# Optimization experiments

Measured on AMD Instinct MI355X. Metric: run time of the kernel, lower is better.

Reference implementation:

```python
import jax, jax.numpy as jnp
import numpy as np

B, C, H, N, M = 4, 256, 4, 2048, 2048
D = C // H  # head_dim
BN_EPS = 1e-5


def conv1x1(W, b, x):
    # nn.Conv1d(Cin, Cout, kernel_size=1): x [B, Cin, N] -> [B, Cout, N]
    return jnp.einsum('oc,bcn->bon', W, x) + b[None, :, None]


def setup_inputs() -> dict:
    key = jax.random.key(0)
    ks = jax.random.split(key, 10)
    w = lambda k, shape: (jax.random.normal(k, shape, jnp.float32) * 0.05)
    return {
        'x1': jax.random.normal(ks[0], (B, C, N), jnp.float32),
        'x2': jax.random.normal(ks[1], (B, C, M), jnp.float32),
        'kv_mask': jax.random.randint(ks[2], (B, M), 0, 2).astype(bool),
        'Wq': w(ks[3], (C, C)), 'bq': jnp.zeros((C,), jnp.float32),
        'Wk': w(ks[4], (C, C)), 'bk': jnp.zeros((C,), jnp.float32),
        'Wv': w(ks[5], (C, C)), 'bv': jnp.zeros((C,), jnp.float32),
        'Wmh': w(ks[6], (C, C)), 'bmh': jnp.zeros((C,), jnp.float32),
        'W1': w(ks[7], (2 * C, 2 * C)), 'b1': jnp.zeros((2 * C,), jnp.float32),
        'bn_gamma': jnp.ones((2 * C,), jnp.float32),
        'bn_beta': jnp.zeros((2 * C,), jnp.float32),
        'bn_mean': jnp.zeros((2 * C,), jnp.float32),
        'bn_var': jnp.ones((2 * C,), jnp.float32),
        'W2': w(ks[8], (C, 2 * C)), 'b2': jnp.zeros((C,), jnp.float32),
    }


def reference(x1, x2, kv_mask, Wq, bq, Wk, bk, Wv, bv, Wmh, bmh,
              W1, b1, bn_gamma, bn_beta, bn_mean, bn_var, W2, b2):
    bsz = x1.shape[0]
    # 1x1-conv Q/K/V projections, reshaped to [B, H, D, N]
    q = conv1x1(Wq, bq, x1).reshape(bsz, H, D, -1)
    k = conv1x1(Wk, bk, x2).reshape(bsz, H, D, -1)
    v = conv1x1(Wv, bv, x2).reshape(bsz, H, D, -1)

    # full attention: scores [B, H, N, M]
    QK = jnp.einsum('bhdn,bhdm->bhnm', q, k)
    # masked_fill happens BEFORE the 1/sqrt(D) scaling in the original
    QK = jnp.where(kv_mask[:, None, None, :], QK, jnp.float32(-1e6))
    score = jax.nn.softmax(QK / np.float32(np.sqrt(D)), axis=-1)
    add_value = jnp.einsum('bhnm,bhdm->bhdn', score, v).reshape(bsz, H * D, -1)

    add_value = conv1x1(Wmh, bmh, add_value)

    # cat_filter: conv1x1 -> BatchNorm1d (inference stats) -> ReLU -> conv1x1
    cat = jnp.concatenate([x1, add_value], axis=1)  # [B, 2C, N]
    h = conv1x1(W1, b1, cat)
    h = (h - bn_mean[None, :, None]) / jnp.sqrt(bn_var[None, :, None] + BN_EPS)
    h = bn_gamma[None, :, None] * h + bn_beta[None, :, None]
    h = jax.nn.relu(h)
    return x1 + conv1x1(W2, b2, h)
```

## Files before the change

kernel.cpp:

```cpp
#include <hip/hip_runtime.h>
#include <hip/hip_bf16.h>

#define SEQN 2048
#define SEQM 2048
#define CDIM 256
#define NB   4
#define NH   4

using bf16x8 = __attribute__((ext_vector_type(8))) short;
using f32x4  = __attribute__((ext_vector_type(4))) float;

__device__ inline unsigned short f2bf(float x) {
    __hip_bfloat16 h = __float2bfloat16(x);
    return *reinterpret_cast<unsigned short*>(&h);
}

__global__ __launch_bounds__(256) void prep_k(
    const int* __restrict__ kvm, int* __restrict__ pidx, int* __restrict__ mcnt,
    const float* __restrict__ W1, const float* __restrict__ b1,
    const float* __restrict__ gamma, const float* __restrict__ beta,
    const float* __restrict__ mean, const float* __restrict__ var,
    const float* __restrict__ Wmh, const float* __restrict__ bmh,
    unsigned short* __restrict__ Acat, float* __restrict__ cvec,
    const float* __restrict__ Wq, const float* __restrict__ Wk,
    const float* __restrict__ Wv, const float* __restrict__ W2,
    unsigned short* __restrict__ Wqb, unsigned short* __restrict__ Wkb,
    unsigned short* __restrict__ Wvb, unsigned short* __restrict__ W2b,
    const float* __restrict__ x1, const float* __restrict__ x2,
    unsigned short* __restrict__ catT, unsigned short* __restrict__ x2T)
{
    __shared__ float smemf[64 * 68];
    const int bid = blockIdx.x, tid = threadIdx.x;

    if (bid < NB) {
        int* sc = reinterpret_cast<int*>(smemf);
        const int b = bid;
        int loc[8], c = 0;
        #pragma unroll
        for (int e = 0; e < 8; ++e) {
            loc[e] = (kvm[(size_t)b * SEQM + tid * 8 + e] != 0) ? 1 : 0;
            c += loc[e];
        }
        sc[tid] = c;
        __syncthreads();
        for (int off = 1; off < 256; off <<= 1) {
            int v = (tid >= off) ? sc[tid - off] : 0;
            __syncthreads();
            sc[tid] += v;
            __syncthreads();
        }
        int p = sc[tid] - c;
        if (tid == 255) mcnt[b] = sc[255];
        #pragma unroll
        for (int e = 0; e < 8; ++e) {
            pidx[(size_t)b * SEQM + tid * 8 + e] = loc[e] ? p : -1;
            p += loc[e];
        }
    } else if (bid < NB + 512) {
        const int j = bid - NB;
        const int c = tid;
        const float s = gamma[j] * rsqrtf(var[j] + 1e-5f);
        const float* w1b = W1 + (size_t)j * 512 + 256;
        Acat[(size_t)j * 512 + c] = f2bf(s * W1[(size_t)j * 512 + c]);
        float acc = 0.f;
        for (int t = 0; t < 256; ++t)
            acc += w1b[t] * Wmh[(size_t)t * 256 + c];
        Acat[(size_t)j * 512 + 256 + c] = f2bf(s * acc);
        if (c == 0) {
            float ab = 0.f;
            for (int t = 0; t < 256; ++t) ab += w1b[t] * bmh[t];
            cvec[j] = s * (b1[j] + ab - mean[j]) + beta[j];
        }
    } else if (bid < NB + 512 + 320) {
        int cid = bid - (NB + 512);
        const float* src; unsigned short* dst; int n;
        if (cid < 64)       { src = Wq; dst = Wqb; n = 65536; }
        else if (cid < 128) { src = Wk; dst = Wkb; n = 65536;  cid -= 64;  }
        else if (cid < 192) { src = Wv; dst = Wvb; n = 65536;  cid -= 128; }
        else                { src = W2; dst = W2b; n = 131072; cid -= 192; }
        const int idx = (cid * 256 + tid) * 4;
        if (idx < n) {
            float4 v = *reinterpret_cast<const float4*>(&src[idx]);
            ushort4 p; p.x = f2bf(v.x); p.y = f2bf(v.y); p.z = f2bf(v.z); p.w = f2bf(v.w);
            *reinterpret_cast<ushort4*>(&dst[idx]) = p;
        }
    } else {
        int t = bid - (NB + 512 + 320);
        const float* src; unsigned short* dst; int ldd;
        if (t < 512) { src = x1; dst = catT; ldd = 512; }
        else         { src = x2; dst = x2T;  ldd = 256; t -= 512; }
        const int cx = t & 3, ny = (t >> 2) & 31, b = t >> 7;
        const int c0 = cx * 64, n0 = ny * 64;
        float (*Ts)[68] = reinterpret_cast<float(*)[68]>(smemf);
        const int cr = tid >> 2, nc = (tid & 3) * 16;
        #pragma unroll
        for (int q = 0; q < 4; ++q) {
            float4 v = *reinterpret_cast<const float4*>(
                &src[((size_t)b * CDIM + c0 + cr) * SEQN + n0 + nc + 4 * q]);
            *reinterpret_cast<float4*>(&Ts[cr][nc + 4 * q]) = v;
        }
        __syncthreads();
        const int nr = tid >> 2, cc = (tid & 3) * 16;
        unsigned short tmp[16];
        #pragma unroll
        for (int e = 0; e < 16; ++e) tmp[e] = f2bf(Ts[cc + e][nr]);
        unsigned short* dp = &dst[((size_t)(b * SEQN + n0 + nr)) * ldd + c0 + cc];
        #pragma unroll
        for (int q = 0; q < 4; ++q)
            *reinterpret_cast<ushort4*>(&dp[4 * q]) = *reinterpret_cast<ushort4*>(&tmp[4 * q]);
    }
}

__global__ __launch_bounds__(256) void qkv_gemm_k(
    const unsigned short* __restrict__ Wqb, const unsigned short* __restrict__ Wkb,
    const unsigned short* __restrict__ Wvb,
    const unsigned short* __restrict__ catT, const unsigned short* __restrict__ x2T,
    const float* __restrict__ bq, const float* __restrict__ bk,
    const float* __restrict__ bv,
    unsigned short* __restrict__ qbf, unsigned short* __restrict__ kbf,
    unsigned short* __restrict__ vbf,
    const int* __restrict__ pidx, float qscale)
{
    __shared__ short At[128][72];
    __shared__ short Bt[64][72];
    const int z = blockIdx.z;
    const unsigned short* W = (z == 0) ? Wqb : (z == 1) ? Wkb : Wvb;
    const unsigned short* X = (z == 0) ? catT : x2T;
    const float* bias = (z == 0) ? bq : (z == 1) ? bk : bv;
    const int ldx = (z == 0) ? 512 : 256;

    const int tid = threadIdx.x;
    const int w = tid >> 6, l = tid & 63, lm = l & 15, lg = l >> 4;
    const int o0 = blockIdx.x * 128, ng0 = blockIdx.y * 64;
    const int wo = (w >> 1) * 64, wn = (w & 1) * 32;

    f32x4 acc[4][2] = {};
    const int arow = tid >> 2, acol = (tid & 3) * 16;

    for (int k0 = 0; k0 < 256; k0 += 64) {
        __syncthreads();
        #pragma unroll
        for (int p = 0; p < 2; ++p) {
            const unsigned short* s = &W[(size_t)(o0 + arow + 64 * p) * 256 + k0 + acol];
            *reinterpret_cast<bf16x8*>(&At[arow + 64 * p][acol]) =
                *reinterpret_cast<const bf16x8*>(s);
            *reinterpret_cast<bf16x8*>(&At[arow + 64 * p][acol + 8]) =
                *reinterpret_cast<const bf16x8*>(s + 8);
        }
        {
            const unsigned short* s = &X[(size_t)(ng0 + arow) * ldx + k0 + acol];
            *reinterpret_cast<bf16x8*>(&Bt[arow][acol]) =
                *reinterpret_cast<const bf16x8*>(s);
            *reinterpret_cast<bf16x8*>(&Bt[arow][acol + 8]) =
                *reinterpret_cast<const bf16x8*>(s + 8);
        }
        __syncthreads();
        #pragma unroll
        for (int kc = 0; kc < 2; ++kc) {
            bf16x8 a[4], bf[2];
            #pragma unroll
            for (int i = 0; i < 4; ++i)
                a[i] = *reinterpret_cast<const bf16x8*>(&At[wo + 16 * i + lm][kc * 32 + lg * 8]);
            #pragma unroll
            for (int j = 0; j < 2; ++j)
                bf[j] = *reinterpret_cast<const bf16x8*>(&Bt[wn + 16 * j + lm][kc * 32 + lg * 8]);
            #pragma unroll
            for (int i = 0; i < 4; ++i)
                #pragma unroll
                for (int j = 0; j < 2; ++j)
                    acc[i][j] = __builtin_amdgcn_mfma_f32_16x16x32_bf16(a[i], bf[j], acc[i][j], 0, 0, 0);
        }
    }

    #pragma unroll
    for (int j = 0; j < 2; ++j) {
        const int ng = ng0 + wn + 16 * j + lm;
        const int b = ng >> 11, n = ng & 2047;
        const int pos = (z == 0) ? n : pidx[(size_t)b * SEQM + n];
        #pragma unroll
        for (int i = 0; i < 4; ++i) {
            const int ob = o0 + wo + 16 * i + 4 * lg;
            float4 bv4 = *reinterpret_cast<const float4*>(&bias[ob]);
            float v[4] = {acc[i][j][0] + bv4.x, acc[i][j][1] + bv4.y,
                          acc[i][j][2] + bv4.z, acc[i][j][3] + bv4.w};
            if (z == 2) {
                if (pos >= 0) {
                    #pragma unroll
                    for (int r = 0; r < 4; ++r)
                        vbf[((size_t)b * CDIM + ob + r) * SEQM + pos] = f2bf(v[r]);
                }
            } else if (pos >= 0) {
                const int hh = ob >> 6, dbase = ob & 63;
                const float sc_ = (z == 0) ? qscale : 1.0f;
                ushort4 pk;
                pk.x = f2bf(v[0] * sc_); pk.y = f2bf(v[1] * sc_);
                pk.z = f2bf(v[2] * sc_); pk.w = f2bf(v[3] * sc_);
                unsigned short* dst = (z == 0) ? qbf : kbf;
                *reinterpret_cast<ushort4*>(
                    &dst[(((size_t)b * NH + hh) * SEQN + pos) * 64 + dbase]) = pk;
            }
        }
    }
}

template<int OMODE>
__global__ __launch_bounds__(256) void gemm_mfma_k(
    const unsigned short* __restrict__ W, const unsigned short* __restrict__ X,
    const float* __restrict__ bias, const float* __restrict__ res,
    unsigned short* __restrict__ obf, float* __restrict__ ofp,
    const int* __restrict__ pidx, int K, int ldx, float oscale)
{
    __shared__ short At[128][72];
    __shared__ short Bt[64][72];
    const int tid = threadIdx.x;
    const int w = tid >> 6, l = tid & 63, lm = l & 15, lg = l >> 4;
    const int o0 = blockIdx.x * 128, ng0 = blockIdx.y * 64;
    const int wo = (w >> 1) * 64, wn = (w & 1) * 32;

    f32x4 acc[4][2] = {};
    const int arow = tid >> 2, acol = (tid & 3) * 16;

    for (int k0 = 0; k0 < K; k0 += 64) {
        __syncthreads();
        #pragma unroll
        for (int p = 0; p < 2; ++p) {
            const unsigned short* s = &W[(size_t)(o0 + arow + 64 * p) * K + k0 + acol];
            *reinterpret_cast<bf16x8*>(&At[arow + 64 * p][acol]) =
                *reinterpret_cast<const bf16x8*>(s);
            *reinterpret_cast<bf16x8*>(&At[arow + 64 * p][acol + 8]) =
                *reinterpret_cast<const bf16x8*>(s + 8);
        }
        {
            const unsigned short* s = &X[(size_t)(ng0 + arow) * ldx + k0 + acol];
            *reinterpret_cast<bf16x8*>(&Bt[arow][acol]) =
                *reinterpret_cast<const bf16x8*>(s);
            *reinterpret_cast<bf16x8*>(&Bt[arow][acol + 8]) =
                *reinterpret_cast<const bf16x8*>(s + 8);
        }
        __syncthreads();
        #pragma unroll
        for (int kc = 0; kc < 2; ++kc) {
            bf16x8 a[4], bf[2];
            #pragma unroll
            for (int i = 0; i < 4; ++i)
                a[i] = *reinterpret_cast<const bf16x8*>(&At[wo + 16 * i + lm][kc * 32 + lg * 8]);
            #pragma unroll
            for (int j = 0; j < 2; ++j)
                bf[j] = *reinterpret_cast<const bf16x8*>(&Bt[wn + 16 * j + lm][kc * 32 + lg * 8]);
            #pragma unroll
            for (int i = 0; i < 4; ++i)
                #pragma unroll
                for (int j = 0; j < 2; ++j)
                    acc[i][j] = __builtin_amdgcn_mfma_f32_16x16x32_bf16(a[i], bf[j], acc[i][j], 0, 0, 0);
        }
    }

    #pragma unroll
    for (int j = 0; j < 2; ++j) {
        const int ng = ng0 + wn + 16 * j + lm;
        const int b = ng >> 11, n = ng & 2047;
        #pragma unroll
        for (int i = 0; i < 4; ++i) {
            const int ob = o0 + wo + 16 * i + 4 * lg;
            float4 bv = *reinterpret_cast<const float4*>(&bias[ob]);
            float v[4] = {acc[i][j][0] + bv.x, acc[i][j][1] + bv.y,
                          acc[i][j][2] + bv.z, acc[i][j][3] + bv.w};
            if (OMODE == 2) {
                ushort4 pk;
                pk.x = f2bf(fmaxf(v[0], 0.f)); pk.y = f2bf(fmaxf(v[1], 0.f));
                pk.z = f2bf(fmaxf(v[2], 0.f)); pk.w = f2bf(fmaxf(v[3], 0.f));
                *reinterpret_cast<ushort4*>(&obf[(size_t)ng * 512 + ob]) = pk;
            } else {
                #pragma unroll
                for (int r = 0; r < 4; ++r) {
                    size_t ad = ((size_t)b * CDIM + ob + r) * SEQN + n;
                    ofp[ad] = v[r] + res[ad];
                }
            }
        }
    }
}

__global__ __launch_bounds__(256) void attn_mfma_k(
    const unsigned short* __restrict__ qbf, const unsigned short* __restrict__ kbf,
    const unsigned short* __restrict__ vbf, const int* __restrict__ mcntg,
    unsigned short* __restrict__ catT)
{
    __shared__ short Ks[2][64][64];
    __shared__ short Vs[2][64][64];
    __shared__ unsigned int Ps[4][16][36];

    const int tid = threadIdx.x;
    const int w = tid >> 6, l = tid & 63;
    const int lm = l & 15, lg = l >> 4;
    const int h = blockIdx.y, b = blockIdx.z;
    const int n_base = blockIdx.x * 64 + w * 16;
    const size_t bhN = (size_t)(b * NH + h) * SEQN;
    const size_t cBase = (size_t)b * CDIM + h * 64;

    const int mcnt = mcntg[b];
    const int ntiles = (mcnt + 63) >> 6;

    if (ntiles == 0) {
        #pragma unroll
        for (int r = 0; r < 4; ++r) {
            int n = n_base + 4 * lg + r;
            unsigned short* dst = &catT[((size_t)b * SEQN + n) * 512 + 256 + h * 64];
            #pragma unroll
            for (int t = 0; t < 4; ++t) dst[16 * t + lm] = 0;
        }
        return;
    }

    const size_t qrow = (bhN + n_base + lm) * 64;
    bf16x8 qa0 = *reinterpret_cast<const bf16x8*>(&qbf[qrow + lg * 8]);
    bf16x8 qa1 = *reinterpret_cast<const bf16x8*>(&qbf[qrow + 32 + lg * 8]);

    f32x4 oacc[4] = {};
    float mrun = -3.0e5f, lrun = 0.f;

    const int r0 = tid >> 3, c8 = (tid & 7) * 8;
    const int c8s = c8 ^ ((r0 & 7) << 3);
    const int colr0 = (lg * 8) ^ ((lm & 7) << 3);
    const int colr1 = (32 + lg * 8) ^ ((lm & 7) << 3);

    {
        bf16x8 kr[2], vr[2];
        #pragma unroll
        for (int p = 0; p < 2; ++p) {
            kr[p] = *reinterpret_cast<const bf16x8*>(&kbf[(bhN + r0 + 32 * p) * 64 + c8]);
            vr[p] = *reinterpret_cast<const bf16x8*>(&vbf[(cBase + r0 + 32 * p) * SEQM + c8]);
        }
        #pragma unroll
        for (int p = 0; p < 2; ++p) {
            *reinterpret_cast<bf16x8*>(&Ks[0][r0 + 32 * p][c8s]) = kr[p];
            *reinterpret_cast<bf16x8*>(&Vs[0][r0 + 32 * p][c8s]) = vr[p];
        }
    }
    __syncthreads();

    for (int t64 = 0; t64 < ntiles; ++t64) {
        const int cur = t64 & 1;
        const bool has_next = (t64 < ntiles - 1);
        const int m0n = (t64 + 1) * 64;

        bf16x8 kr[2], vr[2];
        if (has_next) {
            #pragma unroll
            for (int p = 0; p < 2; ++p) {
                kr[p] = *reinterpret_cast<const bf16x8*>(
                    &kbf[(bhN + m0n + r0 + 32 * p) * 64 + c8]);
                vr[p] = *reinterpret_cast<const bf16x8*>(
                    &vbf[(cBase + r0 + 32 * p) * SEQM + m0n + c8]);
            }
        }

        f32x4 sv[4];
        __builtin_amdgcn_s_setprio(1);
        #pragma unroll
        for (int t = 0; t < 4; ++t) {
            bf16x8 ka0 = *reinterpret_cast<const bf16x8*>(&Ks[cur][16 * t + lm][colr0]);
            bf16x8 ka1 = *reinterpret_cast<const bf16x8*>(&Ks[cur][16 * t + lm][colr1]);
            f32x4 z = {0.f, 0.f, 0.f, 0.f};
            z = __builtin_amdgcn_mfma_f32_16x16x32_bf16(ka0, qa0, z, 0, 0, 0);
            z = __builtin_amdgcn_mfma_f32_16x16x32_bf16(ka1, qa1, z, 0, 0, 0);
            sv[t] = z;
        }
        __builtin_amdgcn_s_setprio(0);

        float mx = fmaxf(fmaxf(fmaxf(sv[0][0], sv[0][1]), fmaxf(sv[0][2], sv[0][3])),
                         fmaxf(fmaxf(sv[1][0], sv[1][1]), fmaxf(sv[1][2], sv[1][3])));
        mx = fmaxf(mx, fmaxf(fmaxf(fmaxf(sv[2][0], sv[2][1]), fmaxf(sv[2][2], sv[2][3])),
                             fmaxf(fmaxf(sv[3][0], sv[3][1]), fmaxf(sv[3][2], sv[3][3]))));
        mx = fmaxf(mx, __shfl_xor(mx, 16));
        mx = fmaxf(mx, __shfl_xor(mx, 32));
        const bool grew = (mx > mrun);
        float mnew = fmaxf(mrun, mx);
        float scl = exp2f(mrun - mnew);
        mrun = mnew;

        float rsum = 0.f;
        const int mrem = mcnt - t64 * 64;
        if (mrem >= 64) {
            #pragma unroll
            for (int t = 0; t < 4; ++t) {
                float p0 = exp2f(sv[t][0] - mnew);
                float p1 = exp2f(sv[t][1] - mnew);
                float p2 = exp2f(sv[t][2] - mnew);
                float p3 = exp2f(sv[t][3] - mnew);
                rsum += (p0 + p1) + (p2 + p3);
                unsigned int u0 = __builtin_amdgcn_perm(
                    __float_as_uint(p1), __float_as_uint(p0), 0x07060302u);
                unsigned int u1 = __builtin_amdgcn_perm(
                    __float_as_uint(p3), __float_as_uint(p2), 0x07060302u);
                *reinterpret_cast<uint2*>(&Ps[w][lm][8 * t + 2 * lg]) = make_uint2(u0, u1);
            }
        } else {
            #pragma unroll
            for (int t = 0; t < 4; ++t) {
                const int mb = 16 * t + 4 * lg;
                float p0 = (mb + 0 < mrem) ? exp2f(sv[t][0] - mnew) : 0.f;
                float p1 = (mb + 1 < mrem) ? exp2f(sv[t][1] - mnew) : 0.f;
                float p2 = (mb + 2 < mrem) ? exp2f(sv[t][2] - mnew) : 0.f;
                float p3 = (mb + 3 < mrem) ? exp2f(sv[t][3] - mnew) : 0.f;
                rsum += (p0 + p1) + (p2 + p3);
                unsigned int u0 = __builtin_amdgcn_perm(
                    __float_as_uint(p1), __float_as_uint(p0), 0x07060302u);
                unsigned int u1 = __builtin_amdgcn_perm(
                    __float_as_uint(p3), __float_as_uint(p2), 0x07060302u);
                *reinterpret_cast<uint2*>(&Ps[w][lm][8 * t + 2 * lg]) = make_uint2(u0, u1);
            }
        }
        rsum += __shfl_xor(rsum, 16);
        rsum += __shfl_xor(rsum, 32);
        lrun = lrun * scl + rsum;

        if (__any(grew && scl < 1.f)) {
            float sr[4];
            #pragma unroll
            for (int r = 0; r < 4; ++r) sr[r] = __shfl(scl, 4 * lg + r);
            #pragma unroll
            for (int t = 0; t < 4; ++t)
                #pragma unroll
                for (int r = 0; r < 4; ++r)
                    oacc[t][r] *= sr[r];
        }

        bf16x8 pa0 = *reinterpret_cast<const bf16x8*>(&Ps[w][lm][4 * lg]);
        bf16x8 pa1 = *reinterpret_cast<const bf16x8*>(&Ps[w][lm][16 + 4 * lg]);
        __builtin_amdgcn_s_setprio(1);
        #pragma unroll
        for (int t = 0; t < 4; ++t) {
            bf16x8 vb0 = *reinterpret_cast<const bf16x8*>(&Vs[cur][16 * t + lm][colr0]);
            bf16x8 vb1 = *reinterpret_cast<const bf16x8*>(&Vs[cur][16 * t + lm][colr1]);
            oacc[t] = __builtin_amdgcn_mfma_f32_16x16x32_bf16(pa0, vb0, oacc[t], 0, 0, 0);
            oacc[t] = __builtin_amdgcn_mfma_f32_16x16x32_bf16(pa1, vb1, oacc[t], 0, 0, 0);
        }
        __builtin_amdgcn_s_setprio(0);

        if (has_next) {
            const int nxt = cur ^ 1;
            #pragma unroll
            for (int p = 0; p < 2; ++p) {
                *reinterpret_cast<bf16x8*>(&Ks[nxt][r0 + 32 * p][c8s]) = kr[p];
                *reinterpret_cast<bf16x8*>(&Vs[nxt][r0 + 32 * p][c8s]) = vr[p];
            }
        }
        __syncthreads();
    }

    #pragma unroll
    for (int r = 0; r < 4; ++r) {
        float rinv = 1.f / __shfl(lrun, 4 * lg + r);
        int n = n_base + 4 * lg + r;
        unsigned short* dst = &catT[((size_t)b * SEQN + n) * 512 + 256 + h * 64];
        #pragma unroll
        for (int t = 0; t < 4; ++t)
            dst[16 * t + lm] = f2bf(oacc[t][r] * rinv);
    }
}

extern "C" void kernel_launch(void* const* d_in, const int* in_sizes, int n_in,
                              void* d_out, int out_size, void* d_ws, size_t ws_size,
                              hipStream_t stream)
{
    (void)in_sizes; (void)n_in; (void)out_size; (void)ws_size;
    const float* x1    = (const float*)d_in[0];
    const float* x2    = (const float*)d_in[1];
    const int*   kvm   = (const int*)  d_in[2];
    const float* Wq    = (const float*)d_in[3];
    const float* bq    = (const float*)d_in[4];
    const float* Wk    = (const float*)d_in[5];
    const float* bk    = (const float*)d_in[6];
    const float* Wv    = (const float*)d_in[7];
    const float* bv    = (const float*)d_in[8];
    const float* Wmh   = (const float*)d_in[9];
    const float* bmh   = (const float*)d_in[10];
    const float* W1    = (const float*)d_in[11];
    const float* b1    = (const float*)d_in[12];
    const float* gamma = (const float*)d_in[13];
    const float* beta  = (const float*)d_in[14];
    const float* mean  = (const float*)d_in[15];
    const float* var   = (const float*)d_in[16];
    const float* W2    = (const float*)d_in[17];
    const float* b2    = (const float*)d_in[18];
    float* out = (float*)d_out;

    const size_t act = (size_t)NB * CDIM * SEQN;
    unsigned short* ws   = (unsigned short*)d_ws;
    unsigned short* qbf  = ws;
    unsigned short* kbf  = qbf  + act;
    unsigned short* vbf  = kbf  + act;
    unsigned short* x2T  = vbf  + act;
    unsigned short* catT = x2T  + act;
    unsigned short* hbuf = catT + 2 * act;
    unsigned short* Wqb  = hbuf + 2 * act;
    unsigned short* Wkb  = Wqb  + 65536;
    unsigned short* Wvb  = Wkb  + 65536;
    unsigned short* W2b  = Wvb  + 65536;
    unsigned short* Acat = W2b  + 131072;
    float*          cvec = (float*)(Acat + 262144);
    int*            pidx = (int*)(cvec + 512);
    int*            mcnt = pidx + (size_t)NB * SEQM;

    const float qscale = 0.125f * 1.44269504088896f;

    prep_k<<<dim3(NB + 512 + 320 + 1024), dim3(256), 0, stream>>>(
        kvm, pidx, mcnt,
        W1, b1, gamma, beta, mean, var, Wmh, bmh, Acat, cvec,
        Wq, Wk, Wv, W2, Wqb, Wkb, Wvb, W2b,
        x1, x2, catT, x2T);

    qkv_gemm_k<<<dim3(2, 128, 3), dim3(256), 0, stream>>>(
        Wqb, Wkb, Wvb, catT, x2T, bq, bk, bv, qbf, kbf, vbf, pidx, qscale);

    attn_mfma_k<<<dim3(SEQN / 64, NH, NB), dim3(256), 0, stream>>>(
        qbf, kbf, vbf, mcnt, catT);

    gemm_mfma_k<2><<<dim3(4, 128), dim3(256), 0, stream>>>(
        Acat, catT, cvec, nullptr, hbuf, nullptr, nullptr, 512, 512, 1.0f);

    gemm_mfma_k<3><<<dim3(2, 128), dim3(256), 0, stream>>>(
        W2b, hbuf, b2, x1, nullptr, out, nullptr, 512, 512, 1.0f);
}
```

Before: 83.31 us.

## Fuse bf16 conversion into QKV GEMM and merge attention with weight prep

The QKV projection now reads fp32 weights and activations directly, converting to bf16 and transposing through shared memory inside the GEMM. This removes the separate conversion and transpose pass and its intermediate buffers. The mask prefix scan runs in the same launch, and K/V blocks spin on a per-batch ready flag before scattering compacted rows. Attention is merged into one launch with the folded Wmh/W1 weight prep and the W2 conversion, cutting the launch count and letting independent work overlap. The ready flag is never reset between calls, which risks reading stale prefix indices, and the spin-wait depends on the scan blocks being scheduled first.

```diff
diff --git a/kernel.cpp b/kernel.cpp
--- a/kernel.cpp
+++ b/kernel.cpp
@@ -6,6 +6,7 @@
 #define CDIM 256
 #define NB   4
 #define NH   4
+#define RDYMAGIC 0x7A3F19C5u
 
 using bf16x8 = __attribute__((ext_vector_type(8))) short;
 using f32x4  = __attribute__((ext_vector_type(4))) float;
@@ -15,49 +16,363 @@
     return *reinterpret_cast<unsigned short*>(&h);
 }
 
-__global__ __launch_bounds__(256) void prep_k(
+__global__ __launch_bounds__(256, 4) void qkv_k(
+    const float* __restrict__ Wq, const float* __restrict__ Wk,
+    const float* __restrict__ Wv,
+    const float* __restrict__ x1, const float* __restrict__ x2,
+    const float* __restrict__ bq, const float* __restrict__ bk,
+    const float* __restrict__ bv,
+    unsigned short* __restrict__ qbf, unsigned short* __restrict__ kbf,
+    unsigned short* __restrict__ vbf,
     const int* __restrict__ kvm, int* __restrict__ pidx, int* __restrict__ mcnt,
+    unsigned int* __restrict__ rdy, float qscale)
+{
+    __shared__ __align__(16) char qsm[35840];
+    const int bid = blockIdx.x, tid = threadIdx.x;
+
+    if (bid < NB) {
+        int* sc = reinterpret_cast<int*>(qsm);
+        const int b = bid;
+        int loc[8], c = 0;
+        #pragma unroll
+        for (int e = 0; e < 8; ++e) {
+            loc[e] = (kvm[(size_t)b * SEQM + tid * 8 + e] != 0) ? 1 : 0;
+            c += loc[e];
+        }
+        sc[tid] = c;
+        __syncthreads();
+        for (int off = 1; off < 256; off <<= 1) {
+            int v = (tid >= off) ? sc[tid - off] : 0;
+            __syncthreads();
+            sc[tid] += v;
+            __syncthreads();
+        }
+        int p = sc[tid] - c;
+        if (tid == 255) mcnt[b] = sc[255];
+        #pragma unroll
+        for (int e = 0; e < 8; ++e) {
+            pidx[(size_t)b * SEQM + tid * 8 + e] = loc[e] ? p : -1;
+            p += loc[e];
+        }
+        __threadfence();
+        __syncthreads();
+        if (tid == 0)
+            __hip_atomic_store(&rdy[b], RDYMAGIC, __ATOMIC_RELEASE,
+                               __HIP_MEMORY_SCOPE_AGENT);
+        return;
+    }
+
+    const int g = bid - NB;
+    const int z = g >> 8, t = g & 255;
+    const int bx = t & 1, by = t >> 1;
+
+    short (*At)[72] = reinterpret_cast<short(*)[72]>(qsm);
+    float (*Ts)[68] = reinterpret_cast<float(*)[68]>(qsm + 18432);
+
+    const float* W = (z == 0) ? Wq : (z == 1) ? Wk : Wv;
+    const float* X = (z == 0) ? x1 : x2;
+    const float* bias = (z == 0) ? bq : (z == 1) ? bk : bv;
+
+    const int w = tid >> 6, l = tid & 63, lm = l & 15, lg = l >> 4;
+    const int o0 = bx * 128, ng0 = by * 64;
+    const int b = ng0 >> 11, n0 = ng0 & 2047;
+    const int wo = (w >> 1) * 64, wn = (w & 1) * 32;
+
+    f32x4 acc[4][2] = {};
+    const int arow = tid >> 2, acol = (tid & 3) * 16;
+    const int tr = tid >> 2, tc = (tid & 3) * 16;
+    const int tg = (((tc >> 4) ^ ((tr >> 3) & 3)) << 4);
+
+    for (int k0 = 0; k0 < 256; k0 += 64) {
+        __syncthreads();
+        #pragma unroll
+        for (int p = 0; p < 2; ++p) {
+            const float* s = &W[(size_t)(o0 + arow + 64 * p) * 256 + k0 + acol];
+            unsigned int u[8];
+            #pragma unroll
+            for (int q = 0; q < 4; ++q) {
+                float4 f = *reinterpret_cast<const float4*>(&s[4 * q]);
+                u[2 * q]     = (unsigned int)f2bf(f.x) | ((unsigned int)f2bf(f.y) << 16);
+                u[2 * q + 1] = (unsigned int)f2bf(f.z) | ((unsigned int)f2bf(f.w) << 16);
+            }
+            *reinterpret_cast<uint4*>(&At[arow + 64 * p][acol]) =
+                make_uint4(u[0], u[1], u[2], u[3]);
+            *reinterpret_cast<uint4*>(&At[arow + 64 * p][acol + 8]) =
+                make_uint4(u[4], u[5], u[6], u[7]);
+        }
+        {
+            const float* s = &X[((size_t)b * CDIM + k0 + tr) * SEQN + n0 + tc];
+            #pragma unroll
+            for (int q = 0; q < 4; ++q)
+                *reinterpret_cast<float4*>(&Ts[tr][tg + 4 * q]) =
+                    *reinterpret_cast<const float4*>(&s[4 * q]);
+        }
+        __syncthreads();
+        #pragma unroll
+        for (int kc = 0; kc < 2; ++kc) {
+            bf16x8 a[4], bf[2];
+            #pragma unroll
+            for (int i = 0; i < 4; ++i)
+                a[i] = *reinterpret_cast<const bf16x8*>(&At[wo + 16 * i + lm][kc * 32 + lg * 8]);
+            #pragma unroll
+            for (int j = 0; j < 2; ++j) {
+                const int bk0 = kc * 32 + lg * 8;
+                const int gcol = (((((wn >> 4) + j)) ^ ((bk0 >> 3) & 3)) << 4) | lm;
+                union { unsigned int u[4]; bf16x8 v; } cv;
+                #pragma unroll
+                for (int e = 0; e < 4; ++e) {
+                    float lo = Ts[bk0 + 2 * e][gcol];
+                    float hi = Ts[bk0 + 2 * e + 1][gcol];
+                    cv.u[e] = (unsigned int)f2bf(lo) | ((unsigned int)f2bf(hi) << 16);
+                }
+                bf[j] = cv.v;
+            }
+            #pragma unroll
+            for (int i = 0; i < 4; ++i)
+                #pragma unroll
+                for (int j = 0; j < 2; ++j)
+                    acc[i][j] = __builtin_amdgcn_mfma_f32_16x16x32_bf16(a[i], bf[j], acc[i][j], 0, 0, 0);
+        }
+    }
+
+    if (z != 0) {
+        if (tid == 0) {
+            while (__hip_atomic_load(&rdy[b], __ATOMIC_ACQUIRE,
+                                     __HIP_MEMORY_SCOPE_AGENT) != RDYMAGIC)
+                __builtin_amdgcn_s_sleep(2);
+        }
+        __syncthreads();
+    }
+
+    #pragma unroll
+    for (int j = 0; j < 2; ++j) {
+        const int ng = ng0 + wn + 16 * j + lm;
+        const int bb = ng >> 11, n = ng & 2047;
+        const int pos = (z == 0) ? n : pidx[(size_t)bb * SEQM + n];
+        #pragma unroll
+        for (int i = 0; i < 4; ++i) {
+            const int ob = o0 + wo + 16 * i + 4 * lg;
+            float4 bv4 = *reinterpret_cast<const float4*>(&bias[ob]);
+            float v[4] = {acc[i][j][0] + bv4.x, acc[i][j][1] + bv4.y,
+                          acc[i][j][2] + bv4.z, acc[i][j][3] + bv4.w};
+            if (z == 2) {
+                if (pos >= 0) {
+                    #pragma unroll
+                    for (int r = 0; r < 4; ++r)
+                        vbf[((size_t)bb * CDIM + ob + r) * SEQM + pos] = f2bf(v[r]);
+                }
+            } else if (pos >= 0) {
+                const int hh = ob >> 6, dbase = ob & 63;
+                const float sc_ = (z == 0) ? qscale : 1.0f;
+                ushort4 pk;
+                pk.x = f2bf(v[0] * sc_); pk.y = f2bf(v[1] * sc_);
+                pk.z = f2bf(v[2] * sc_); pk.w = f2bf(v[3] * sc_);
+                unsigned short* dst = (z == 0) ? qbf : kbf;
+                *reinterpret_cast<ushort4*>(
+                    &dst[(((size_t)bb * NH + hh) * SEQN + pos) * 64 + dbase]) = pk;
+            }
+        }
+    }
+}
+
+__device__ void do_attn(char* smraw,
+    const unsigned short* __restrict__ qbf, const unsigned short* __restrict__ kbf,
+    const unsigned short* __restrict__ vbf, const int* __restrict__ mcntg,
+    unsigned short* __restrict__ catT, int bx, int h, int b)
+{
+    short (*Ks)[64][64] = reinterpret_cast<short(*)[64][64]>(smraw);
+    short (*Vs)[64][64] = reinterpret_cast<short(*)[64][64]>(smraw + 16384);
+    unsigned int (*Ps)[16][36] = reinterpret_cast<unsigned int(*)[16][36]>(smraw + 32768);
+
+    const int tid = threadIdx.x;
+    const int w = tid >> 6, l = tid & 63;
+    const int lm = l & 15, lg = l >> 4;
+    const int n_base = bx * 64 + w * 16;
+    const size_t bhN = (size_t)(b * NH + h) * SEQN;
+    const size_t cBase = (size_t)b * CDIM + h * 64;
+
+    const int mcnt = mcntg[b];
+    const int ntiles = (mcnt + 63) >> 6;
+
+    if (ntiles == 0) {
+        #pragma unroll
+        for (int r = 0; r < 4; ++r) {
+            int n = n_base + 4 * lg + r;
+            unsigned short* dst = &catT[((size_t)b * SEQN + n) * 512 + 256 + h * 64];
+            #pragma unroll
+            for (int t = 0; t < 4; ++t) dst[16 * t + lm] = 0;
+        }
+        return;
+    }
+
+    const size_t qrow = (bhN + n_base + lm) * 64;
+    bf16x8 qa0 = *reinterpret_cast<const bf16x8*>(&qbf[qrow + lg * 8]);
+    bf16x8 qa1 = *reinterpret_cast<const bf16x8*>(&qbf[qrow + 32 + lg * 8]);
+
+    f32x4 oacc[4] = {};
+    float mrun = -3.0e5f, lrun = 0.f;
+
+    const int r0 = tid >> 3, c8 = (tid & 7) * 8;
+    const int c8s = c8 ^ ((r0 & 7) << 3);
+    const int colr0 = (lg * 8) ^ ((lm & 7) << 3);
+    const int colr1 = (32 + lg * 8) ^ ((lm & 7) << 3);
+
+    {
+        bf16x8 kr[2], vr[2];
+        #pragma unroll
+        for (int p = 0; p < 2; ++p) {
+            kr[p] = *reinterpret_cast<const bf16x8*>(&kbf[(bhN + r0 + 32 * p) * 64 + c8]);
+            vr[p] = *reinterpret_cast<const bf16x8*>(&vbf[(cBase + r0 + 32 * p) * SEQM + c8]);
+        }
+        #pragma unroll
+        for (int p = 0; p < 2; ++p) {
+            *reinterpret_cast<bf16x8*>(&Ks[0][r0 + 32 * p][c8s]) = kr[p];
+            *reinterpret_cast<bf16x8*>(&Vs[0][r0 + 32 * p][c8s]) = vr[p];
+        }
+    }
+    __syncthreads();
+
+    for (int t64 = 0; t64 < ntiles; ++t64) {
+        const int cur = t64 & 1;
+        const bool has_next = (t64 < ntiles - 1);
+        const int m0n = (t64 + 1) * 64;
+
+        bf16x8 kr[2], vr[2];
+        if (has_next) {
+            #pragma unroll
+            for (int p = 0; p < 2; ++p) {
+                kr[p] = *reinterpret_cast<const bf16x8*>(
+                    &kbf[(bhN + m0n + r0 + 32 * p) * 64 + c8]);
+                vr[p] = *reinterpret_cast<const bf16x8*>(
+                    &vbf[(cBase + r0 + 32 * p) * SEQM + m0n + c8]);
+            }
+        }
+
+        f32x4 sv[4];
+        __builtin_amdgcn_s_setprio(1);
+        #pragma unroll
+        for (int t = 0; t < 4; ++t) {
+            bf16x8 ka0 = *reinterpret_cast<const bf16x8*>(&Ks[cur][16 * t + lm][colr0]);
+            bf16x8 ka1 = *reinterpret_cast<const bf16x8*>(&Ks[cur][16 * t + lm][colr1]);
+            f32x4 z = {0.f, 0.f, 0.f, 0.f};
+            z = __builtin_amdgcn_mfma_f32_16x16x32_bf16(ka0, qa0, z, 0, 0, 0);
+            z = __builtin_amdgcn_mfma_f32_16x16x32_bf16(ka1, qa1, z, 0, 0, 0);
+            sv[t] = z;
+        }
+        __builtin_amdgcn_s_setprio(0);
+
+        float mx = fmaxf(fmaxf(fmaxf(sv[0][0], sv[0][1]), fmaxf(sv[0][2], sv[0][3])),
+                         fmaxf(fmaxf(sv[1][0], sv[1][1]), fmaxf(sv[1][2], sv[1][3])));
+        mx = fmaxf(mx, fmaxf(fmaxf(fmaxf(sv[2][0], sv[2][1]), fmaxf(sv[2][2], sv[2][3])),
+                             fmaxf(fmaxf(sv[3][0], sv[3][1]), fmaxf(sv[3][2], sv[3][3]))));
+        mx = fmaxf(mx, __shfl_xor(mx, 16));
+        mx = fmaxf(mx, __shfl_xor(mx, 32));
+        const bool grew = (mx > mrun);
+        float mnew = fmaxf(mrun, mx);
+        float scl = exp2f(mrun - mnew);
+        mrun = mnew;
+
+        float rsum = 0.f;
+        const int mrem = mcnt - t64 * 64;
+        if (mrem >= 64) {
+            #pragma unroll
+            for (int t = 0; t < 4; ++t) {
+                float p0 = exp2f(sv[t][0] - mnew);
+                float p1 = exp2f(sv[t][1] - mnew);
+                float p2 = exp2f(sv[t][2] - mnew);
+                float p3 = exp2f(sv[t][3] - mnew);
+                rsum += (p0 + p1) + (p2 + p3);
+                unsigned int u0 = __builtin_amdgcn_perm(
+                    __float_as_uint(p1), __float_as_uint(p0), 0x07060302u);
+                unsigned int u1 = __builtin_amdgcn_perm(
+                    __float_as_uint(p3), __float_as_uint(p2), 0x07060302u);
+                *reinterpret_cast<uint2*>(&Ps[w][lm][8 * t + 2 * lg]) = make_uint2(u0, u1);
+            }
+        } else {
+            #pragma unroll
+            for (int t = 0; t < 4; ++t) {
+                const int mb = 16 * t + 4 * lg;
+                float p0 = (mb + 0 < mrem) ? exp2f(sv[t][0] - mnew) : 0.f;
+                float p1 = (mb + 1 < mrem) ? exp2f(sv[t][1] - mnew) : 0.f;
+                float p2 = (mb + 2 < mrem) ? exp2f(sv[t][2] - mnew) : 0.f;
+                float p3 = (mb + 3 < mrem) ? exp2f(sv[t][3] - mnew) : 0.f;
+                rsum += (p0 + p1) + (p2 + p3);
+                unsigned int u0 = __builtin_amdgcn_perm(
+                    __float_as_uint(p1), __float_as_uint(p0), 0x07060302u);
+                unsigned int u1 = __builtin_amdgcn_perm(
+                    __float_as_uint(p3), __float_as_uint(p2), 0x07060302u);
+                *reinterpret_cast<uint2*>(&Ps[w][lm][8 * t + 2 * lg]) = make_uint2(u0, u1);
+            }
+        }
+        rsum += __shfl_xor(rsum, 16);
+        rsum += __shfl_xor(rsum, 32);
+        lrun = lrun * scl + rsum;
+
+        if (__any(grew && scl < 1.f)) {
+            float sr[4];
+            #pragma unroll
+            for (int r = 0; r < 4; ++r) sr[r] = __shfl(scl, 4 * lg + r);
+            #pragma unroll
+            for (int t = 0; t < 4; ++t)
+                #pragma unroll
+                for (int r = 0; r < 4; ++r)
+                    oacc[t][r] *= sr[r];
+        }
+
+        bf16x8 pa0 = *reinterpret_cast<const bf16x8*>(&Ps[w][lm][4 * lg]);
+        bf16x8 pa1 = *reinterpret_cast<const bf16x8*>(&Ps[w][lm][16 + 4 * lg]);
+        __builtin_amdgcn_s_setprio(1);
+        #pragma unroll
+        for (int t = 0; t < 4; ++t) {
+            bf16x8 vb0 = *reinterpret_cast<const bf16x8*>(&Vs[cur][16 * t + lm][colr0]);
+            bf16x8 vb1 = *reinterpret_cast<const bf16x8*>(&Vs[cur][16 * t + lm][colr1]);
+            oacc[t] = __builtin_amdgcn_mfma_f32_16x16x32_bf16(pa0, vb0, oacc[t], 0, 0, 0);
+            oacc[t] = __builtin_amdgcn_mfma_f32_16x16x32_bf16(pa1, vb1, oacc[t], 0, 0, 0);
+        }
+        __builtin_amdgcn_s_setprio(0);
+
+        if (has_next) {
+            const int nxt = cur ^ 1;
+            #pragma unroll
+            for (int p = 0; p < 2; ++p) {
+                *reinterpret_cast<bf16x8*>(&Ks[nxt][r0 + 32 * p][c8s]) = kr[p];
+                *reinterpret_cast<bf16x8*>(&Vs[nxt][r0 + 32 * p][c8s]) = vr[p];
+            }
+        }
+        __syncthreads();
+    }
+
+    #pragma unroll
+    for (int r = 0; r < 4; ++r) {
+        float rinv = 1.f / __shfl(lrun, 4 * lg + r);
+        int n = n_base + 4 * lg + r;
+        unsigned short* dst = &catT[((size_t)b * SEQN + n) * 512 + 256 + h * 64];
+        #pragma unroll
+        for (int t = 0; t < 4; ++t)
+            dst[16 * t + lm] = f2bf(oacc[t][r] * rinv);
+    }
+}
+
+__global__ __launch_bounds__(256) void fused2_k(
+    const unsigned short* __restrict__ qbf, const unsigned short* __restrict__ kbf,
+    const unsigned short* __restrict__ vbf, const int* __restrict__ mcnt,
+    unsigned short* __restrict__ catT,
     const float* __restrict__ W1, const float* __restrict__ b1,
     const float* __restrict__ gamma, const float* __restrict__ beta,
     const float* __restrict__ mean, const float* __restrict__ var,
     const float* __restrict__ Wmh, const float* __restrict__ bmh,
     unsigned short* __restrict__ Acat, float* __restrict__ cvec,
-    const float* __restrict__ Wq, const float* __restrict__ Wk,
-    const float* __restrict__ Wv, const float* __restrict__ W2,
-    unsigned short* __restrict__ Wqb, unsigned short* __restrict__ Wkb,
-    unsigned short* __restrict__ Wvb, unsigned short* __restrict__ W2b,
-    const float* __restrict__ x1, const float* __restrict__ x2,
-    unsigned short* __restrict__ catT, unsigned short* __restrict__ x2T)
+    const float* __restrict__ x1,
+    const float* __restrict__ W2, unsigned short* __restrict__ W2b)
 {
-    __shared__ float smemf[64 * 68];
+    __shared__ __align__(16) char smraw[41984];
     const int bid = blockIdx.x, tid = threadIdx.x;
 
-    if (bid < NB) {
-        int* sc = reinterpret_cast<int*>(smemf);
-        const int b = bid;
-        int loc[8], c = 0;
-        #pragma unroll
-        for (int e = 0; e < 8; ++e) {
-            loc[e] = (kvm[(size_t)b * SEQM + tid * 8 + e] != 0) ? 1 : 0;
-            c += loc[e];
-        }
-        sc[tid] = c;
-        __syncthreads();
-        for (int off = 1; off < 256; off <<= 1) {
-            int v = (tid >= off) ? sc[tid - off] : 0;
-            __syncthreads();
-            sc[tid] += v;
-            __syncthreads();
-        }
-        int p = sc[tid] - c;
-        if (tid == 255) mcnt[b] = sc[255];
-        #pragma unroll
-        for (int e = 0; e < 8; ++e) {
-            pidx[(size_t)b * SEQM + tid * 8 + e] = loc[e] ? p : -1;
-            p += loc[e];
-        }
-    } else if (bid < NB + 512) {
-        const int j = bid - NB;
+    if (bid < 512) {
+        do_attn(smraw, qbf, kbf, vbf, mcnt, catT,
+                bid & 31, (bid >> 5) & 3, bid >> 7);
+    } else if (bid < 1024) {
+        const int j = bid - 512;
         const int c = tid;
         const float s = gamma[j] * rsqrtf(var[j] + 1e-5f);
         const float* w1b = W1 + (size_t)j * 512 + 256;
@@ -71,32 +386,16 @@
             for (int t = 0; t < 256; ++t) ab += w1b[t] * bmh[t];
             cvec[j] = s * (b1[j] + ab - mean[j]) + beta[j];
         }
-    } else if (bid < NB + 512 + 320) {
-        int cid = bid - (NB + 512);
-        const float* src; unsigned short* dst; int n;
-        if (cid < 64)       { src = Wq; dst = Wqb; n = 65536; }
-        else if (cid < 128) { src = Wk; dst = Wkb; n = 65536;  cid -= 64;  }
-        else if (cid < 192) { src = Wv; dst = Wvb; n = 65536;  cid -= 128; }
-        else                { src = W2; dst = W2b; n = 131072; cid -= 192; }
-        const int idx = (cid * 256 + tid) * 4;
-        if (idx < n) {
-            float4 v = *reinterpret_cast<const float4*>(&src[idx]);
-            ushort4 p; p.x = f2bf(v.x); p.y = f2bf(v.y); p.z = f2bf(v.z); p.w = f2bf(v.w);
-            *reinterpret_cast<ushort4*>(&dst[idx]) = p;
-        }
-    } else {
-        int t = bid - (NB + 512 + 320);
-        const float* src; unsigned short* dst; int ldd;
-        if (t < 512) { src = x1; dst = catT; ldd = 512; }
-        else         { src = x2; dst = x2T;  ldd = 256; t -= 512; }
+    } else if (bid < 1536) {
+        const int t = bid - 1024;
+        float (*Ts)[68] = reinterpret_cast<float(*)[68]>(smraw);
         const int cx = t & 3, ny = (t >> 2) & 31, b = t >> 7;
         const int c0 = cx * 64, n0 = ny * 64;
-        float (*Ts)[68] = reinterpret_cast<float(*)[68]>(smemf);
         const int cr = tid >> 2, nc = (tid & 3) * 16;
         #pragma unroll
         for (int q = 0; q < 4; ++q) {
             float4 v = *reinterpret_cast<const float4*>(
-                &src[((size_t)b * CDIM + c0 + cr) * SEQN + n0 + nc + 4 * q]);
+                &x1[((size_t)b * CDIM + c0 + cr) * SEQN + n0 + nc + 4 * q]);
             *reinterpret_cast<float4*>(&Ts[cr][nc + 4 * q]) = v;
         }
         __syncthreads();
@@ -104,102 +403,16 @@
         unsigned short tmp[16];
         #pragma unroll
         for (int e = 0; e < 16; ++e) tmp[e] = f2bf(Ts[cc + e][nr]);
-        unsigned short* dp = &dst[((size_t)(b * SEQN + n0 + nr)) * ldd + c0 + cc];
+        unsigned short* dp = &catT[((size_t)(b * SEQN + n0 + nr)) * 512 + c0 + cc];
         #pragma unroll
         for (int q = 0; q < 4; ++q)
             *reinterpret_cast<ushort4*>(&dp[4 * q]) = *reinterpret_cast<ushort4*>(&tmp[4 * q]);
-    }
-}
-
-__global__ __launch_bounds__(256) void qkv_gemm_k(
-    const unsigned short* __restrict__ Wqb, const unsigned short* __restrict__ Wkb,
-    const unsigned short* __restrict__ Wvb,
-    const unsigned short* __restrict__ catT, const unsigned short* __restrict__ x2T,
-    const float* __restrict__ bq, const float* __restrict__ bk,
-    const float* __restrict__ bv,
-    unsigned short* __restrict__ qbf, unsigned short* __restrict__ kbf,
-    unsigned short* __restrict__ vbf,
-    const int* __restrict__ pidx, float qscale)
-{
-    __shared__ short At[128][72];
-    __shared__ short Bt[64][72];
-    const int z = blockIdx.z;
-    const unsigned short* W = (z == 0) ? Wqb : (z == 1) ? Wkb : Wvb;
-    const unsigned short* X = (z == 0) ? catT : x2T;
-    const float* bias = (z == 0) ? bq : (z == 1) ? bk : bv;
-    const int ldx = (z == 0) ? 512 : 256;
-
-    const int tid = threadIdx.x;
-    const int w = tid >> 6, l = tid & 63, lm = l & 15, lg = l >> 4;
-    const int o0 = blockIdx.x * 128, ng0 = blockIdx.y * 64;
-    const int wo = (w >> 1) * 64, wn = (w & 1) * 32;
-
-    f32x4 acc[4][2] = {};
-    const int arow = tid >> 2, acol = (tid & 3) * 16;
-
-    for (int k0 = 0; k0 < 256; k0 += 64) {
-        __syncthreads();
-        #pragma unroll
-        for (int p = 0; p < 2; ++p) {
-            const unsigned short* s = &W[(size_t)(o0 + arow + 64 * p) * 256 + k0 + acol];
-            *reinterpret_cast<bf16x8*>(&At[arow + 64 * p][acol]) =
-                *reinterpret_cast<const bf16x8*>(s);
-            *reinterpret_cast<bf16x8*>(&At[arow + 64 * p][acol + 8]) =
-                *reinterpret_cast<const bf16x8*>(s + 8);
-        }
-        {
-            const unsigned short* s = &X[(size_t)(ng0 + arow) * ldx + k0 + acol];
-            *reinterpret_cast<bf16x8*>(&Bt[arow][acol]) =
-                *reinterpret_cast<const bf16x8*>(s);
-            *reinterpret_cast<bf16x8*>(&Bt[arow][acol + 8]) =
-                *reinterpret_cast<const bf16x8*>(s + 8);
-        }
-        __syncthreads();
-        #pragma unroll
-        for (int kc = 0; kc < 2; ++kc) {
-            bf16x8 a[4], bf[2];
-            #pragma unroll
-            for (int i = 0; i < 4; ++i)
-                a[i] = *reinterpret_cast<const bf16x8*>(&At[wo + 16 * i + lm][kc * 32 + lg * 8]);
-            #pragma unroll
-            for (int j = 0; j < 2; ++j)
-                bf[j] = *reinterpret_cast<const bf16x8*>(&Bt[wn + 16 * j + lm][kc * 32 + lg * 8]);
-            #pragma unroll
-            for (int i = 0; i < 4; ++i)
-                #pragma unroll
-                for (int j = 0; j < 2; ++j)
-                    acc[i][j] = __builtin_amdgcn_mfma_f32_16x16x32_bf16(a[i], bf[j], acc[i][j], 0, 0, 0);
-        }
-    }
-
-    #pragma unroll
-    for (int j = 0; j < 2; ++j) {
-        const int ng = ng0 + wn + 16 * j + lm;
-        const int b = ng >> 11, n = ng & 2047;
-        const int pos = (z == 0) ? n : pidx[(size_t)b * SEQM + n];
-        #pragma unroll
-        for (int i = 0; i < 4; ++i) {
-            const int ob = o0 + wo + 16 * i + 4 * lg;
-            float4 bv4 = *reinterpret_cast<const float4*>(&bias[ob]);
-            float v[4] = {acc[i][j][0] + bv4.x, acc[i][j][1] + bv4.y,
-                          acc[i][j][2] + bv4.z, acc[i][j][3] + bv4.w};
-            if (z == 2) {
-                if (pos >= 0) {
-                    #pragma unroll
-                    for (int r = 0; r < 4; ++r)
-                        vbf[((size_t)b * CDIM + ob + r) * SEQM + pos] = f2bf(v[r]);
-                }
-            } else if (pos >= 0) {
-                const int hh = ob >> 6, dbase = ob & 63;
-                const float sc_ = (z == 0) ? qscale : 1.0f;
-                ushort4 pk;
-                pk.x = f2bf(v[0] * sc_); pk.y = f2bf(v[1] * sc_);
-                pk.z = f2bf(v[2] * sc_); pk.w = f2bf(v[3] * sc_);
-                unsigned short* dst = (z == 0) ? qbf : kbf;
-                *reinterpret_cast<ushort4*>(
-                    &dst[(((size_t)b * NH + hh) * SEQN + pos) * 64 + dbase]) = pk;
-            }
-        }
+    } else {
+        const int cid = bid - 1536;
+        const int idx = (cid * 256 + tid) * 4;
+        float4 v = *reinterpret_cast<const float4*>(&W2[idx]);
+        ushort4 p; p.x = f2bf(v.x); p.y = f2bf(v.y); p.z = f2bf(v.z); p.w = f2bf(v.w);
+        *reinterpret_cast<ushort4*>(&W2b[idx]) = p;
     }
 }
 
@@ -208,7 +421,7 @@
     const unsigned short* __restrict__ W, const unsigned short* __restrict__ X,
     const float* __restrict__ bias, const float* __restrict__ res,
     unsigned short* __restrict__ obf, float* __restrict__ ofp,
-    const int* __restrict__ pidx, int K, int ldx, float oscale)
+    int K, int ldx)
 {
     __shared__ short At[128][72];
     __shared__ short Bt[64][72];
@@ -278,185 +491,6 @@
                 }
             }
         }
-    }
-}
-
-__global__ __launch_bounds__(256) void attn_mfma_k(
-    const unsigned short* __restrict__ qbf, const unsigned short* __restrict__ kbf,
-    const unsigned short* __restrict__ vbf, const int* __restrict__ mcntg,
-    unsigned short* __restrict__ catT)
-{
-    __shared__ short Ks[2][64][64];
-    __shared__ short Vs[2][64][64];
-    __shared__ unsigned int Ps[4][16][36];
-
-    const int tid = threadIdx.x;
-    const int w = tid >> 6, l = tid & 63;
-    const int lm = l & 15, lg = l >> 4;
-    const int h = blockIdx.y, b = blockIdx.z;
-    const int n_base = blockIdx.x * 64 + w * 16;
-    const size_t bhN = (size_t)(b * NH + h) * SEQN;
-    const size_t cBase = (size_t)b * CDIM + h * 64;
-
-    const int mcnt = mcntg[b];
-    const int ntiles = (mcnt + 63) >> 6;
-
-    if (ntiles == 0) {
-        #pragma unroll
-        for (int r = 0; r < 4; ++r) {
-            int n = n_base + 4 * lg + r;
-            unsigned short* dst = &catT[((size_t)b * SEQN + n) * 512 + 256 + h * 64];
-            #pragma unroll
-            for (int t = 0; t < 4; ++t) dst[16 * t + lm] = 0;
-        }
-        return;
-    }
-
-    const size_t qrow = (bhN + n_base + lm) * 64;
-    bf16x8 qa0 = *reinterpret_cast<const bf16x8*>(&qbf[qrow + lg * 8]);
-    bf16x8 qa1 = *reinterpret_cast<const bf16x8*>(&qbf[qrow + 32 + lg * 8]);
-
-    f32x4 oacc[4] = {};
-    float mrun = -3.0e5f, lrun = 0.f;
-
-    const int r0 = tid >> 3, c8 = (tid & 7) * 8;
-    const int c8s = c8 ^ ((r0 & 7) << 3);
-    const int colr0 = (lg * 8) ^ ((lm & 7) << 3);
-    const int colr1 = (32 + lg * 8) ^ ((lm & 7) << 3);
-
-    {
-        bf16x8 kr[2], vr[2];
-        #pragma unroll
-        for (int p = 0; p < 2; ++p) {
-            kr[p] = *reinterpret_cast<const bf16x8*>(&kbf[(bhN + r0 + 32 * p) * 64 + c8]);
-            vr[p] = *reinterpret_cast<const bf16x8*>(&vbf[(cBase + r0 + 32 * p) * SEQM + c8]);
-        }
-        #pragma unroll
-        for (int p = 0; p < 2; ++p) {
-            *reinterpret_cast<bf16x8*>(&Ks[0][r0 + 32 * p][c8s]) = kr[p];
-            *reinterpret_cast<bf16x8*>(&Vs[0][r0 + 32 * p][c8s]) = vr[p];
-        }
-    }
-    __syncthreads();
-
-    for (int t64 = 0; t64 < ntiles; ++t64) {
-        const int cur = t64 & 1;
-        const bool has_next = (t64 < ntiles - 1);
-        const int m0n = (t64 + 1) * 64;
-
-        bf16x8 kr[2], vr[2];
-        if (has_next) {
-            #pragma unroll
-            for (int p = 0; p < 2; ++p) {
-                kr[p] = *reinterpret_cast<const bf16x8*>(
-                    &kbf[(bhN + m0n + r0 + 32 * p) * 64 + c8]);
-                vr[p] = *reinterpret_cast<const bf16x8*>(
-                    &vbf[(cBase + r0 + 32 * p) * SEQM + m0n + c8]);
-            }
-        }
-
-        f32x4 sv[4];
-        __builtin_amdgcn_s_setprio(1);
-        #pragma unroll
-        for (int t = 0; t < 4; ++t) {
-            bf16x8 ka0 = *reinterpret_cast<const bf16x8*>(&Ks[cur][16 * t + lm][colr0]);
-            bf16x8 ka1 = *reinterpret_cast<const bf16x8*>(&Ks[cur][16 * t + lm][colr1]);
-            f32x4 z = {0.f, 0.f, 0.f, 0.f};
-            z = __builtin_amdgcn_mfma_f32_16x16x32_bf16(ka0, qa0, z, 0, 0, 0);
-            z = __builtin_amdgcn_mfma_f32_16x16x32_bf16(ka1, qa1, z, 0, 0, 0);
-            sv[t] = z;
-        }
-        __builtin_amdgcn_s_setprio(0);
-
-        float mx = fmaxf(fmaxf(fmaxf(sv[0][0], sv[0][1]), fmaxf(sv[0][2], sv[0][3])),
-                         fmaxf(fmaxf(sv[1][0], sv[1][1]), fmaxf(sv[1][2], sv[1][3])));
-        mx = fmaxf(mx, fmaxf(fmaxf(fmaxf(sv[2][0], sv[2][1]), fmaxf(sv[2][2], sv[2][3])),
-                             fmaxf(fmaxf(sv[3][0], sv[3][1]), fmaxf(sv[3][2], sv[3][3]))));
-        mx = fmaxf(mx, __shfl_xor(mx, 16));
-        mx = fmaxf(mx, __shfl_xor(mx, 32));
-        const bool grew = (mx > mrun);
-        float mnew = fmaxf(mrun, mx);
-        float scl = exp2f(mrun - mnew);
-        mrun = mnew;
-
-        float rsum = 0.f;
-        const int mrem = mcnt - t64 * 64;
-        if (mrem >= 64) {
-            #pragma unroll
-            for (int t = 0; t < 4; ++t) {
-                float p0 = exp2f(sv[t][0] - mnew);
-                float p1 = exp2f(sv[t][1] - mnew);
-                float p2 = exp2f(sv[t][2] - mnew);
-                float p3 = exp2f(sv[t][3] - mnew);
-                rsum += (p0 + p1) + (p2 + p3);
-                unsigned int u0 = __builtin_amdgcn_perm(
-                    __float_as_uint(p1), __float_as_uint(p0), 0x07060302u);
-                unsigned int u1 = __builtin_amdgcn_perm(
-                    __float_as_uint(p3), __float_as_uint(p2), 0x07060302u);
-                *reinterpret_cast<uint2*>(&Ps[w][lm][8 * t + 2 * lg]) = make_uint2(u0, u1);
-            }
-        } else {
-            #pragma unroll
-            for (int t = 0; t < 4; ++t) {
-                const int mb = 16 * t + 4 * lg;
-                float p0 = (mb + 0 < mrem) ? exp2f(sv[t][0] - mnew) : 0.f;
-                float p1 = (mb + 1 < mrem) ? exp2f(sv[t][1] - mnew) : 0.f;
-                float p2 = (mb + 2 < mrem) ? exp2f(sv[t][2] - mnew) : 0.f;
-                float p3 = (mb + 3 < mrem) ? exp2f(sv[t][3] - mnew) : 0.f;
-                rsum += (p0 + p1) + (p2 + p3);
-                unsigned int u0 = __builtin_amdgcn_perm(
-                    __float_as_uint(p1), __float_as_uint(p0), 0x07060302u);
-                unsigned int u1 = __builtin_amdgcn_perm(
-                    __float_as_uint(p3), __float_as_uint(p2), 0x07060302u);
-                *reinterpret_cast<uint2*>(&Ps[w][lm][8 * t + 2 * lg]) = make_uint2(u0, u1);
-            }
-        }
-        rsum += __shfl_xor(rsum, 16);
-        rsum += __shfl_xor(rsum, 32);
-        lrun = lrun * scl + rsum;
-
-        if (__any(grew && scl < 1.f)) {
-            float sr[4];
-            #pragma unroll
-            for (int r = 0; r < 4; ++r) sr[r] = __shfl(scl, 4 * lg + r);
-            #pragma unroll
-            for (int t = 0; t < 4; ++t)
-                #pragma unroll
-                for (int r = 0; r < 4; ++r)
-                    oacc[t][r] *= sr[r];
-        }
-
-        bf16x8 pa0 = *reinterpret_cast<const bf16x8*>(&Ps[w][lm][4 * lg]);
-        bf16x8 pa1 = *reinterpret_cast<const bf16x8*>(&Ps[w][lm][16 + 4 * lg]);
-        __builtin_amdgcn_s_setprio(1);
-        #pragma unroll
-        for (int t = 0; t < 4; ++t) {
-            bf16x8 vb0 = *reinterpret_cast<const bf16x8*>(&Vs[cur][16 * t + lm][colr0]);
-            bf16x8 vb1 = *reinterpret_cast<const bf16x8*>(&Vs[cur][16 * t + lm][colr1]);
-            oacc[t] = __builtin_amdgcn_mfma_f32_16x16x32_bf16(pa0, vb0, oacc[t], 0, 0, 0);
-            oacc[t] = __builtin_amdgcn_mfma_f32_16x16x32_bf16(pa1, vb1, oacc[t], 0, 0, 0);
-        }
-        __builtin_amdgcn_s_setprio(0);
-
-        if (has_next) {
-            const int nxt = cur ^ 1;
-            #pragma unroll
-            for (int p = 0; p < 2; ++p) {
-                *reinterpret_cast<bf16x8*>(&Ks[nxt][r0 + 32 * p][c8s]) = kr[p];
-                *reinterpret_cast<bf16x8*>(&Vs[nxt][r0 + 32 * p][c8s]) = vr[p];
-            }
-        }
-        __syncthreads();
-    }
-
-    #pragma unroll
-    for (int r = 0; r < 4; ++r) {
-        float rinv = 1.f / __shfl(lrun, 4 * lg + r);
-        int n = n_base + 4 * lg + r;
-        unsigned short* dst = &catT[((size_t)b * SEQN + n) * 512 + 256 + h * 64];
-        #pragma unroll
-        for (int t = 0; t < 4; ++t)
-            dst[16 * t + lm] = f2bf(oacc[t][r] * rinv);
     }
 }
 
@@ -487,39 +521,33 @@
     float* out = (float*)d_out;
 
     const size_t act = (size_t)NB * CDIM * SEQN;
-    unsigned short* ws   = (unsigned short*)d_ws;
-    unsigned short* qbf  = ws;
-    unsigned short* kbf  = qbf  + act;
-    unsigned short* vbf  = kbf  + act;
-    unsigned short* x2T  = vbf  + act;
-    unsigned short* catT = x2T  + act;
-    unsigned short* hbuf = catT + 2 * act;
-    unsigned short* Wqb  = hbuf + 2 * act;
-    unsigned short* Wkb  = Wqb  + 65536;
-    unsigned short* Wvb  = Wkb  + 65536;
-    unsigned short* W2b  = Wvb  + 65536;
-    unsigned short* Acat = W2b  + 131072;
-    float*          cvec = (float*)(Acat + 262144);
-    int*            pidx = (int*)(cvec + 512);
-    int*            mcnt = pidx + (size_t)NB * SEQM;
+    unsigned short* ws    = (unsigned short*)d_ws;
+    unsigned short* qbf   = ws;
+    unsigned short* kbf   = qbf   + act;
+    unsigned short* vbf   = kbf   + act;
+    unsigned short* catT  = vbf   + act;
+    unsigned short* hbuf  = catT  + 2 * act;
+    unsigned short* W2b   = hbuf  + 2 * act;
+    unsigned short* Acat  = W2b   + 131072;
+    float*          cvec  = (float*)(Acat + 262144);
+    int*            pidx  = (int*)(cvec + 512);
+    int*            mcnt  = pidx + (size_t)NB * SEQM;
+    unsigned int*   rdy   = (unsigned int*)(mcnt + 16);
 
     const float qscale = 0.125f * 1.44269504088896f;
 
-    prep_k<<<dim3(NB + 512 + 320 + 1024), dim3(256), 0, stream>>>(
-        kvm, pidx, mcnt,
+    qkv_k<<<dim3(NB + 768), dim3(256), 0, stream>>>(
+        Wq, Wk, Wv, x1, x2, bq, bk, bv, qbf, kbf, vbf,
+        kvm, pidx, mcnt, rdy, qscale);
+
+    fused2_k<<<dim3(1664), dim3(256), 0, stream>>>(
+        qbf, kbf, vbf, mcnt, catT,
         W1, b1, gamma, beta, mean, var, Wmh, bmh, Acat, cvec,
-        Wq, Wk, Wv, W2, Wqb, Wkb, Wvb, W2b,
-        x1, x2, catT, x2T);
-
-    qkv_gemm_k<<<dim3(2, 128, 3), dim3(256), 0, stream>>>(
-        Wqb, Wkb, Wvb, catT, x2T, bq, bk, bv, qbf, kbf, vbf, pidx, qscale);
-
-    attn_mfma_k<<<dim3(SEQN / 64, NH, NB), dim3(256), 0, stream>>>(
-        qbf, kbf, vbf, mcnt, catT);
+        x1, W2, W2b);
 
     gemm_mfma_k<2><<<dim3(4, 128), dim3(256), 0, stream>>>(
-        Acat, catT, cvec, nullptr, hbuf, nullptr, nullptr, 512, 512, 1.0f);
+        Acat, catT, cvec, nullptr, hbuf, nullptr, 512, 512);
 
     gemm_mfma_k<3><<<dim3(2, 128), dim3(256), 0, stream>>>(
-        W2b, hbuf, b2, x1, nullptr, out, nullptr, 512, 512, 1.0f);
+        W2b, hbuf, b2, x1, nullptr, out, 512, 512);
 }
```

New measurement: 78.12 us. 1.07x faster.
